# Performance work log

Hardware: AMD Instinct MI355X
Metric: run time of the kernel (lower is better)

## Reference

```python
import math
import jax, jax.numpy as jnp
import numpy as np

N_INPUTS, N_OUTPUTS = 2049, 1024
OUT_START, OUT_END, IN_END = 25.0, 24000.0, 24000.0


def _build_buffers(n_inputs=N_INPUTS, n_outputs=N_OUTPUTS, output_start=OUT_START,
                   output_end=OUT_END, input_end=IN_END):
    # Mirrors LogScale.__init__ (numpy, construction-time, exact).
    scale = 1.0
    min_log = math.log10(1.0 + scale * output_start)
    max_log = math.log10(1.0 + scale * output_end)
    lin_logs = np.linspace(min_log, max_log, n_outputs, dtype=np.float64)
    freq_per_bin = scale * float(input_end) / (n_inputs - 1)
    center_bins = ((np.power(10.0, lin_logs) - 1.0) / freq_per_bin).astype(np.float32)
    n_linear = 0
    while n_linear < n_outputs - 1 and (center_bins[n_linear + 1] - center_bins[n_linear] <= 1.0 or center_bins[n_linear] < 1.0):
        n_linear += 1
    output_start_idx = center_bins[:n_linear].astype(np.int64)
    fraction_linear = center_bins[:n_linear] - output_start_idx.astype(np.float32)
    linear_pair_idx = (np.concatenate([output_start_idx, output_start_idx + 1])
                       if n_linear > 0 else np.zeros(0, dtype=np.int64))
    n_sum = n_linear
    while n_sum < n_outputs - 2 and (center_bins[n_sum + 1] - center_bins[n_sum] <= 2.0 or center_bins[n_sum] < 2.0):
        n_sum += 1
    fraction_cubic = center_bins[n_linear:n_sum].copy()
    n_tri = n_outputs - n_sum
    ft = center_bins[n_sum:n_sum + n_tri]
    dt = center_bins[n_sum:n_sum + n_tri] - center_bins[n_sum - 1:n_sum - 1 + n_tri]
    weights = np.full((max(n_tri, 1), n_inputs), -np.inf, dtype=np.float32)
    for i in range(n_tri):
        i_mid = int(math.ceil(ft[i]))
        i_start = int(math.ceil(ft[i] - dt[i]))
        i_end = int(math.ceil(ft[i] + dt[i + 1])) if i < n_tri - 1 else i_mid
        weights[i, i_mid] = 0.0
        dist_left = float(i_mid - i_start)
        for ib in range(i_start + 1, i_mid):
            weights[i, ib] = np.float32(10.0 * np.log10(1.0 - (i_mid - ib) / dist_left))
        if i_end > i_mid:
            dist_right = float(i_end - i_mid)
            for ib in range(i_mid + 1, i_end):
                weights[i, ib] = np.float32(10.0 * np.log10(np.float32(1.0 - (ib - i_mid) / dist_right)))
    return linear_pair_idx, fraction_linear, fraction_cubic, weights[:n_tri]


def setup_inputs() -> dict:
    key = jax.random.key(0)
    x = jax.random.normal(key, (32, 512, N_INPUTS), dtype=jnp.float32)
    pidx, flin, fcub, w = _build_buffers()
    return {
        "x": x,
        "fraction_linear": jnp.asarray(flin),
        "fraction_cubic": jnp.asarray(fcub),
        "triangular_weights": jnp.asarray(w),
        "linear_pair_idx": jnp.asarray(pidx, dtype=jnp.int32),
    }


_TRI_CHUNK = 128  # rows of flattened x per lax.map step (bounds the dense intermediate)


def _tri_max(flat, w):
    # (x[:, None, :] + w).max(-1), chunked along N to keep the (chunk, n_tri, n_in)
    # intermediate bounded, mirroring the torch _triangular_amax chunking.
    n, n_in = flat.shape
    pad = (-n) % _TRI_CHUNK
    flat_p = jnp.pad(flat, ((0, pad), (0, 0)))
    xb = flat_p.reshape(-1, _TRI_CHUNK, n_in)
    out = jax.lax.map(lambda xc: jnp.max(xc[:, None, :] + w[None, :, :], axis=-1), xb)
    return out.reshape(-1, w.shape[0])[:n]


def _forward(x, fraction_linear, fraction_cubic, triangular_weights, linear_pair_idx):
    lead = x.shape[:-1]
    n_lin = fraction_linear.shape[0]
    outs = []
    if n_lin > 0:
        pair = jnp.take(x, linear_pair_idx, axis=-1).reshape(*lead, 2, n_lin)
        x0, x1 = pair[..., 0, :], pair[..., 1, :]
        outs.append(x0 + fraction_linear * (x1 - x0))
    if fraction_cubic.shape[0] > 0:
        i0 = jnp.floor(fraction_cubic).astype(jnp.int32)
        f = fraction_cubic - i0.astype(fraction_cubic.dtype)
        g = lambda off: jnp.take(x, i0 + off, axis=-1)
        xm1, xc0, xc1, xc2 = g(-1), g(0), g(1), g(2)
        # Catmull-Rom cubic interpolation at fractional position f in [0,1)
        cubic = xc0 + 0.5 * f * ((xc1 - xm1) + f * ((2.0 * xm1 - 5.0 * xc0 + 4.0 * xc1 - xc2)
                                                    + f * (3.0 * (xc0 - xc1) + xc2 - xm1)))
        outs.append(cubic)
    if triangular_weights.shape[0] > 0:
        flat = x.reshape(-1, x.shape[-1])
        outs.append(_tri_max(flat, triangular_weights).reshape(*lead, triangular_weights.shape[0]))
    return jnp.concatenate(outs, axis=-1)


def reference(x, fraction_linear, fraction_cubic, triangular_weights, linear_pair_idx):
    return _forward(x, fraction_linear, fraction_cubic, triangular_weights, linear_pair_idx)
```

## Files before the change

kernel.cpp:

```cpp
#include <hip/hip_runtime.h>
#include <math.h>

#define NI 2049
#define ROWS 4
#define WCAP 4096
#define NTRI_MAX 512

__device__ __forceinline__ int pad(int i) { return i + (i >> 5); }
#define XS_SZ (ROWS * NI + (ROWS * NI >> 5) + 4)
#define WL_SZ (WCAP + (WCAP >> 5) + 4)

__global__ void logscale_win(const float* __restrict__ w, int n_in,
                             int* __restrict__ tri_start,
                             int* __restrict__ tri_cnt) {
    const int i = blockIdx.x;
    __shared__ int smin, smax;
    if (threadIdx.x == 0) { smin = n_in; smax = -1; }
    __syncthreads();
    int lmin = n_in, lmax = -1;
    const float* wr = w + (size_t)i * n_in;
    for (int b = threadIdx.x; b < n_in; b += blockDim.x) {
        float v = wr[b];
        if (v > -1e30f) { lmin = min(lmin, b); lmax = max(lmax, b); }
    }
    atomicMin(&smin, lmin);
    atomicMax(&smax, lmax);
    __syncthreads();
    if (threadIdx.x == 0) {
        int s = smin, cnt = smax - smin + 1;
        if (cnt < 1) { s = 0; cnt = 1; }
        if (cnt > 64) cnt = 64;
        tri_start[i] = s; tri_cnt[i] = cnt;
    }
}

__global__ void logscale_pack(const float* __restrict__ w,
                              const float* __restrict__ flin,
                              const float* __restrict__ fcub,
                              const int*   __restrict__ pidx,
                              const int*   __restrict__ tri_start,
                              const int*   __restrict__ tri_cnt,
                              float4* __restrict__ meta,
                              float*  __restrict__ wpk,
                              int*    __restrict__ d_total,
                              int n_lin, int n_cub, int n_tri) {
    __shared__ int offs[NTRI_MAX + 1];
    __shared__ int starts[NTRI_MAX];
    const int tid = threadIdx.x;
    for (int i = tid; i < n_tri; i += blockDim.x) {
        offs[i + 1] = tri_cnt[i];
        starts[i]   = tri_start[i];
    }
    __syncthreads();
    if (tid == 0) {
        offs[0] = 0;
        for (int i = 1; i <= n_tri; ++i) offs[i] += offs[i - 1];
        int t = offs[n_tri]; if (t > WCAP) t = WCAP;
        *d_total = t;
    }
    __syncthreads();
    int total = offs[n_tri]; if (total > WCAP) total = WCAP;

    const int n_out = n_lin + n_cub + n_tri;
    for (int o = tid; o < n_out; o += blockDim.x) {
        float4 m;
        if (o < n_lin) {
            m.x = __int_as_float(pidx[o]);
            m.y = __int_as_float(pidx[n_lin + o]);
            m.z = flin[o]; m.w = 0.0f;
        } else if (o < n_lin + n_cub) {
            float c = fcub[o - n_lin];
            int i0 = (int)floorf(c);
            m.x = __int_as_float(i0);
            m.y = 0.0f;
            m.z = c - (float)i0; m.w = 0.0f;
        } else {
            int i = o - n_lin - n_cub;
            int oa = min(offs[i], WCAP), ob = min(offs[i + 1], WCAP);
            m.x = __int_as_float(starts[i]);
            m.y = __int_as_float(ob - oa);
            m.z = __int_as_float(oa); m.w = 0.0f;
        }
        meta[o] = m;
    }
    for (int p = tid; p < total; p += blockDim.x) {
        int lo = 0, hi = n_tri - 1;
        while (lo < hi) {
            int mid = (lo + hi + 1) >> 1;
            if (offs[mid] <= p) lo = mid; else hi = mid - 1;
        }
        int j = p - offs[lo];
        wpk[p] = w[(size_t)lo * NI + starts[lo] + j];
    }
}

__global__ __launch_bounds__(256) void logscale_main(
    const float*  __restrict__ x,
    const float4* __restrict__ meta,
    const float*  __restrict__ wpk,
    const int*    __restrict__ d_total,
    float* __restrict__ out,
    int n_lin, int n_cub, int n_out, int n_rows) {

    __shared__ float xs[XS_SZ];
    __shared__ float wl[WL_SZ];

    const int tid  = threadIdx.x;
    const int row0 = blockIdx.x * ROWS;
    const int rows_here = min(ROWS, n_rows - row0);

    const float* xr = x + (size_t)row0 * NI;
    const int nx = rows_here * NI;
    for (int i = tid; i < nx; i += 256) xs[pad(i)] = xr[i];
    const int tw = *d_total;
    for (int i = tid; i < tw; i += 256) wl[pad(i)] = wpk[i];
    __syncthreads();

    const int n_lc = n_lin + n_cub;
    float* ob = out + (size_t)row0 * n_out;

    if (rows_here == ROWS) {
        for (int o = tid; o < n_out; o += 256) {
            const float4 m = meta[o];
            float res[ROWS];
            if (o < n_lin) {
                const int i0 = __float_as_int(m.x);
                const int i1 = __float_as_int(m.y);
                const float f = m.z;
                #pragma unroll
                for (int r = 0; r < ROWS; ++r) {
                    const int b = r * NI;
                    const float x0 = xs[pad(b + i0)];
                    const float x1 = xs[pad(b + i1)];
                    res[r] = x0 + f * (x1 - x0);
                }
            } else if (o < n_lc) {
                const int i0 = __float_as_int(m.x);
                const float f = m.z;
                #pragma unroll
                for (int r = 0; r < ROWS; ++r) {
                    const int b = r * NI + i0;
                    const float xm1 = xs[pad(b - 1)];
                    const float x0  = xs[pad(b)];
                    const float x1  = xs[pad(b + 1)];
                    const float x2  = xs[pad(b + 2)];
                    res[r] = x0 + 0.5f * f * (x1 - xm1 +
                             f * (2.0f * xm1 - 5.0f * x0 + 4.0f * x1 - x2 +
                             f * (3.0f * (x0 - x1) + x2 - xm1)));
                }
            } else {
                const int s   = __float_as_int(m.x);
                const int cnt = __float_as_int(m.y);
                const int off = __float_as_int(m.z);
                float acc0 = -INFINITY, acc1 = -INFINITY;
                float acc2 = -INFINITY, acc3 = -INFINITY;
                for (int j = 0; j < cnt; ++j) {
                    const float wj = wl[pad(off + j)];
                    const int b = s + j;
                    acc0 = fmaxf(acc0, xs[pad(b)] + wj);
                    acc1 = fmaxf(acc1, xs[pad(b + NI)] + wj);
                    acc2 = fmaxf(acc2, xs[pad(b + 2 * NI)] + wj);
                    acc3 = fmaxf(acc3, xs[pad(b + 3 * NI)] + wj);
                }
                res[0] = acc0; res[1] = acc1; res[2] = acc2; res[3] = acc3;
            }
            #pragma unroll
            for (int r = 0; r < ROWS; ++r)
                ob[(size_t)r * n_out + o] = res[r];
        }
    } else {
        for (int o = tid; o < n_out; o += 256) {
            const float4 m = meta[o];
            for (int r = 0; r < rows_here; ++r) {
                const int b = r * NI;
                float res;
                if (o < n_lin) {
                    const int i0 = __float_as_int(m.x);
                    const int i1 = __float_as_int(m.y);
                    const float f = m.z;
                    const float x0 = xs[pad(b + i0)];
                    const float x1 = xs[pad(b + i1)];
                    res = x0 + f * (x1 - x0);
                } else if (o < n_lc) {
                    const int i0 = __float_as_int(m.x) + b;
                    const float f = m.z;
                    const float xm1 = xs[pad(i0 - 1)];
                    const float x0  = xs[pad(i0)];
                    const float x1  = xs[pad(i0 + 1)];
                    const float x2  = xs[pad(i0 + 2)];
                    res = x0 + 0.5f * f * (x1 - xm1 +
                          f * (2.0f * xm1 - 5.0f * x0 + 4.0f * x1 - x2 +
                          f * (3.0f * (x0 - x1) + x2 - xm1)));
                } else {
                    const int s   = __float_as_int(m.x) + b;
                    const int cnt = __float_as_int(m.y);
                    const int off = __float_as_int(m.z);
                    float mx = -INFINITY;
                    for (int j = 0; j < cnt; ++j)
                        mx = fmaxf(mx, xs[pad(s + j)] + wl[pad(off + j)]);
                    res = mx;
                }
                ob[(size_t)r * n_out + o] = res;
            }
        }
    }
}

extern "C" void kernel_launch(void* const* d_in, const int* in_sizes, int n_in,
                              void* d_out, int out_size, void* d_ws, size_t ws_size,
                              hipStream_t stream) {
    (void)n_in; (void)ws_size; (void)out_size;
    const float* x    = (const float*)d_in[0];
    const float* flin = (const float*)d_in[1];
    const float* fcub = (const float*)d_in[2];
    const float* w    = (const float*)d_in[3];
    const int*   pidx = (const int*)d_in[4];
    float* out = (float*)d_out;

    const int n_lin  = in_sizes[1];
    const int n_cub  = in_sizes[2];
    const int n_tri  = in_sizes[3] / NI;
    const int n_rows = in_sizes[0] / NI;
    const int n_out  = n_lin + n_cub + n_tri;

    float4* meta      = (float4*)d_ws;
    float*  wpk       = (float*)(meta + n_out);
    int*    tri_start = (int*)(wpk + WCAP);
    int*    tri_cnt   = tri_start + NTRI_MAX;
    int*    d_total   = tri_cnt + NTRI_MAX;

    if (n_tri > 0)
        logscale_win<<<n_tri, 256, 0, stream>>>(w, NI, tri_start, tri_cnt);
    logscale_pack<<<1, 256, 0, stream>>>(w, flin, fcub, pidx, tri_start, tri_cnt,
                                         meta, wpk, d_total, n_lin, n_cub, n_tri);
    const int nblk = (n_rows + ROWS - 1) / ROWS;
    logscale_main<<<nblk, 256, 0, stream>>>(x, meta, wpk, d_total, out,
                                            n_lin, n_cub, n_out, n_rows);
}
```

Baseline: 271.0 us.

## Vectorize shared-memory staging, drop padding, and parallelize pack prefix scan

Removes the bank-conflict padding from the shared arrays so that x rows and packed weights can be staged with float4 loads. The main-kernel inner loops now index shared memory directly, which saves the pad arithmetic on every access. The pack kernel replaces its serial prefix sum with a 64-lane wavefront shuffle scan, and replaces the per-element binary search with one wave per triangle window. Risks: the float4 loads require 16-byte alignment of each row block and of wpk, and the scan only covers n_tri up to 512. Dropping padding may also bring back bank conflicts.

```diff
diff --git a/kernel.cpp b/kernel.cpp
--- a/kernel.cpp
+++ b/kernel.cpp
@@ -5,10 +5,6 @@
 #define ROWS 4
 #define WCAP 4096
 #define NTRI_MAX 512
-
-__device__ __forceinline__ int pad(int i) { return i + (i >> 5); }
-#define XS_SZ (ROWS * NI + (ROWS * NI >> 5) + 4)
-#define WL_SZ (WCAP + (WCAP >> 5) + 4)
 
 __global__ void logscale_win(const float* __restrict__ w, int n_in,
                              int* __restrict__ tri_start,
@@ -51,15 +47,38 @@
         offs[i + 1] = tri_cnt[i];
         starts[i]   = tri_start[i];
     }
+    if (tid == 0) offs[0] = 0;
+    __syncthreads();
+
+    if (tid < 64) {
+        int v[8];
+        int run = 0;
+        const int base = tid * 8;
+        #pragma unroll
+        for (int k = 0; k < 8; ++k) {
+            int idx = base + k;
+            int c = (idx < n_tri) ? offs[idx + 1] : 0;
+            run += c;
+            v[k] = run;
+        }
+        int tot = run;
+        #pragma unroll
+        for (int d = 1; d < 64; d <<= 1) {
+            int up = __shfl_up(tot, (unsigned)d, 64);
+            if (tid >= d) tot += up;
+        }
+        const int excl = tot - run;
+        #pragma unroll
+        for (int k = 0; k < 8; ++k) {
+            int idx = base + k;
+            if (idx < n_tri) offs[idx + 1] = excl + v[k];
+        }
+    }
     __syncthreads();
     if (tid == 0) {
-        offs[0] = 0;
-        for (int i = 1; i <= n_tri; ++i) offs[i] += offs[i - 1];
         int t = offs[n_tri]; if (t > WCAP) t = WCAP;
         *d_total = t;
     }
-    __syncthreads();
-    int total = offs[n_tri]; if (total > WCAP) total = WCAP;
 
     const int n_out = n_lin + n_cub + n_tri;
     for (int o = tid; o < n_out; o += blockDim.x) {
@@ -83,14 +102,13 @@
         }
         meta[o] = m;
     }
-    for (int p = tid; p < total; p += blockDim.x) {
-        int lo = 0, hi = n_tri - 1;
-        while (lo < hi) {
-            int mid = (lo + hi + 1) >> 1;
-            if (offs[mid] <= p) lo = mid; else hi = mid - 1;
-        }
-        int j = p - offs[lo];
-        wpk[p] = w[(size_t)lo * NI + starts[lo] + j];
+
+    const int wv = tid >> 6, ln = tid & 63;
+    for (int i = wv; i < n_tri; i += 4) {
+        const int oa = min(offs[i], WCAP);
+        const int ob = min(offs[i + 1], WCAP);
+        if (ln < ob - oa)
+            wpk[oa + ln] = w[(size_t)i * NI + starts[i] + ln];
     }
 }
 
@@ -102,8 +120,8 @@
     float* __restrict__ out,
     int n_lin, int n_cub, int n_out, int n_rows) {
 
-    __shared__ float xs[XS_SZ];
-    __shared__ float wl[WL_SZ];
+    __shared__ __align__(16) float xs[ROWS * NI];
+    __shared__ __align__(16) float wl[WCAP];
 
     const int tid  = threadIdx.x;
     const int row0 = blockIdx.x * ROWS;
@@ -111,9 +129,17 @@
 
     const float* xr = x + (size_t)row0 * NI;
     const int nx = rows_here * NI;
-    for (int i = tid; i < nx; i += 256) xs[pad(i)] = xr[i];
-    const int tw = *d_total;
-    for (int i = tid; i < tw; i += 256) wl[pad(i)] = wpk[i];
+    const int nq = nx >> 2;
+    const float4* xr4 = (const float4*)xr;
+    float4* xs4 = (float4*)xs;
+    for (int i = tid; i < nq; i += 256) xs4[i] = xr4[i];
+    for (int i = (nq << 2) + tid; i < nx; i += 256) xs[i] = xr[i];
+
+    const int tw  = *d_total;
+    const int twq = (tw + 3) >> 2;
+    const float4* wp4 = (const float4*)wpk;
+    float4* wl4 = (float4*)wl;
+    for (int i = tid; i < twq; i += 256) wl4[i] = wp4[i];
     __syncthreads();
 
     const int n_lc = n_lin + n_cub;
@@ -130,8 +156,8 @@
                 #pragma unroll
                 for (int r = 0; r < ROWS; ++r) {
                     const int b = r * NI;
-                    const float x0 = xs[pad(b + i0)];
-                    const float x1 = xs[pad(b + i1)];
+                    const float x0 = xs[b + i0];
+                    const float x1 = xs[b + i1];
                     res[r] = x0 + f * (x1 - x0);
                 }
             } else if (o < n_lc) {
@@ -140,10 +166,10 @@
                 #pragma unroll
                 for (int r = 0; r < ROWS; ++r) {
                     const int b = r * NI + i0;
-                    const float xm1 = xs[pad(b - 1)];
-                    const float x0  = xs[pad(b)];
-                    const float x1  = xs[pad(b + 1)];
-                    const float x2  = xs[pad(b + 2)];
+                    const float xm1 = xs[b - 1];
+                    const float x0  = xs[b];
+                    const float x1  = xs[b + 1];
+                    const float x2  = xs[b + 2];
                     res[r] = x0 + 0.5f * f * (x1 - xm1 +
                              f * (2.0f * xm1 - 5.0f * x0 + 4.0f * x1 - x2 +
                              f * (3.0f * (x0 - x1) + x2 - xm1)));
@@ -152,15 +178,16 @@
                 const int s   = __float_as_int(m.x);
                 const int cnt = __float_as_int(m.y);
                 const int off = __float_as_int(m.z);
+                const float* wj = wl + off;
+                const float* xp = xs + s;
                 float acc0 = -INFINITY, acc1 = -INFINITY;
                 float acc2 = -INFINITY, acc3 = -INFINITY;
                 for (int j = 0; j < cnt; ++j) {
-                    const float wj = wl[pad(off + j)];
-                    const int b = s + j;
-                    acc0 = fmaxf(acc0, xs[pad(b)] + wj);
-                    acc1 = fmaxf(acc1, xs[pad(b + NI)] + wj);
-                    acc2 = fmaxf(acc2, xs[pad(b + 2 * NI)] + wj);
-                    acc3 = fmaxf(acc3, xs[pad(b + 3 * NI)] + wj);
+                    const float wv = wj[j];
+                    acc0 = fmaxf(acc0, xp[j] + wv);
+                    acc1 = fmaxf(acc1, xp[j + NI] + wv);
+                    acc2 = fmaxf(acc2, xp[j + 2 * NI] + wv);
+                    acc3 = fmaxf(acc3, xp[j + 3 * NI] + wv);
                 }
                 res[0] = acc0; res[1] = acc1; res[2] = acc2; res[3] = acc3;
             }
@@ -178,16 +205,16 @@
                     const int i0 = __float_as_int(m.x);
                     const int i1 = __float_as_int(m.y);
                     const float f = m.z;
-                    const float x0 = xs[pad(b + i0)];
-                    const float x1 = xs[pad(b + i1)];
+                    const float x0 = xs[b + i0];
+                    const float x1 = xs[b + i1];
                     res = x0 + f * (x1 - x0);
                 } else if (o < n_lc) {
                     const int i0 = __float_as_int(m.x) + b;
                     const float f = m.z;
-                    const float xm1 = xs[pad(i0 - 1)];
-                    const float x0  = xs[pad(i0)];
-                    const float x1  = xs[pad(i0 + 1)];
-                    const float x2  = xs[pad(i0 + 2)];
+                    const float xm1 = xs[i0 - 1];
+                    const float x0  = xs[i0];
+                    const float x1  = xs[i0 + 1];
+                    const float x2  = xs[i0 + 2];
                     res = x0 + 0.5f * f * (x1 - xm1 +
                           f * (2.0f * xm1 - 5.0f * x0 + 4.0f * x1 - x2 +
                           f * (3.0f * (x0 - x1) + x2 - xm1)));
@@ -197,7 +224,7 @@
                     const int off = __float_as_int(m.z);
                     float mx = -INFINITY;
                     for (int j = 0; j < cnt; ++j)
-                        mx = fmaxf(mx, xs[pad(s + j)] + wl[pad(off + j)]);
+                        mx = fmaxf(mx, xs[s + j] + wl[off + j]);
                     res = mx;
                 }
                 ob[(size_t)r * n_out + o] = res;
```

Measured after the change: 282.2 us. 4.1% more time.
